# Kernel optimization log

Hardware: AMD Instinct MI355X
Metric: run time of the kernel (lower is better)

Reference implementation:

```python
import jax, jax.numpy as jnp
import numpy as np

DIST_THD = 2.0  # squared-distance threshold from my_chamfer_fn


def setup_inputs() -> dict:
    key = jax.random.key(0)
    k1, k2 = jax.random.split(key)
    pc1 = jax.random.normal(k1, (1, 16384, 3), dtype=jnp.float32)
    pc2 = jax.random.normal(k2, (1, 16384, 3), dtype=jnp.float32)
    return {"pc1": pc1, "pc2": pc2}


def _chamfer(x, y):
    # x: (N, P1, D), y: (N, P2, D). Squared pairwise distances (as pytorch3d knn_points).
    x2 = jnp.sum(x * x, axis=-1)                       # (N, P1)
    y2 = jnp.sum(y * y, axis=-1)                       # (N, P2)
    xy = jnp.einsum('npd,nqd->npq', x, y)              # (N, P1, P2)
    d2 = x2[:, :, None] + y2[:, None, :] - 2.0 * xy    # (N, P1, P2)
    cham_x = jnp.min(d2, axis=2)                       # (N, P1) NN dist x->y (K=1)
    cham_y = jnp.min(d2, axis=1)                       # (N, P2) NN dist y->x
    # threshold mask: distances >= 2 are zeroed
    cham_x = jnp.where(cham_x >= DIST_THD, 0.0, cham_x)
    cham_y = jnp.where(cham_y >= DIST_THD, 0.0, cham_y)
    N, P1, _ = x.shape
    P2 = y.shape[1]
    # point_reduction='mean' (lengths are full P), batch_reduction='mean'
    cx = jnp.sum(cham_x, axis=1) / P1
    cy = jnp.sum(cham_y, axis=1) / P2
    return jnp.sum(cx) / N + jnp.sum(cy) / N


def reference(pc1, pc2):
    # Chamfer loss between pc1 and pc2 (the kernel inside NSFP optimization);
    # normals are unused in this code path, so only the distance loss is returned.
    return _chamfer(pc1, pc2)
```

## Files before the change

### kernel.cpp

```cpp
#include <hip/hip_runtime.h>
#include <hip/hip_bf16.h>


constexpr int P      = 16384;
constexpr int BLK    = 256;
constexpr int NSEG   = 16;
constexpr int SEGPTS = P / NSEG;
constexpr int SEGT   = SEGPTS / 32;
constexpr int ROWSB  = 256;
constexpr int CLOUDB = P * 32;

typedef short s8v  __attribute__((ext_vector_type(8)));
typedef float f16v __attribute__((ext_vector_type(16)));

static __device__ inline unsigned short bf16r(float f) {
    unsigned u = __float_as_uint(f);
    u = (u + 0x7FFFu + ((u >> 16) & 1u)) >> 16;
    return (unsigned short)u;
}
static __device__ inline float bf2f(unsigned short h) {
    return __uint_as_float(((unsigned)h) << 16);
}

static __device__ inline void encA(float a, float b, float c, unsigned e[8]) {
    const unsigned ONE = 0x3F80u;
    const float s = fmaf(a, a, fmaf(b, b, c * c));
    const unsigned short ah = bf16r(a), bh = bf16r(b), ch = bf16r(c);
    const unsigned short al = bf16r(a - bf2f(ah));
    const unsigned short bl = bf16r(b - bf2f(bh));
    const unsigned short cl = bf16r(c - bf2f(ch));
    const unsigned short sh = bf16r(s), sl = bf16r(s - bf2f(sh));
    e[0] = ah | ((unsigned)al << 16);
    e[1] = bh | ((unsigned)bl << 16);
    e[2] = ch | ((unsigned)cl << 16);
    e[3] = ah | ((unsigned)bh << 16);
    e[4] = ch | ((unsigned)sh << 16);
    e[5] = sl | (ONE << 16);
    e[6] = ONE;
    e[7] = 0;
}

static __device__ inline void encB(float a, float b, float c, unsigned e[8]) {
    const unsigned ONE = 0x3F80u;
    const float s = fmaf(a, a, fmaf(b, b, c * c));
    const unsigned short ah = bf16r(a), bh = bf16r(b), ch = bf16r(c);
    const unsigned short al = bf16r(a - bf2f(ah));
    const unsigned short bl = bf16r(b - bf2f(bh));
    const unsigned short cl = bf16r(c - bf2f(ch));
    const unsigned short sh = bf16r(s), sl = bf16r(s - bf2f(sh));
    const unsigned short Ah = bf16r(-2.f * bf2f(ah)), Bh = bf16r(-2.f * bf2f(bh));
    const unsigned short Ch = bf16r(-2.f * bf2f(ch));
    const unsigned short Al = bf16r(-2.f * bf2f(al)), Bl = bf16r(-2.f * bf2f(bl));
    const unsigned short Cl = bf16r(-2.f * bf2f(cl));
    e[0] = Ah | ((unsigned)Ah << 16);
    e[1] = Bh | ((unsigned)Bh << 16);
    e[2] = Ch | ((unsigned)Ch << 16);
    e[3] = Al | ((unsigned)Bl << 16);
    e[4] = Cl | (ONE << 16);
    e[5] = ONE | ((unsigned)sh << 16);
    e[6] = sl;
    e[7] = 0;
}

__global__ __launch_bounds__(BLK) void encode_pts(
    const float* __restrict__ pc1, const float* __restrict__ pc2,
    unsigned char* __restrict__ encAbuf, unsigned char* __restrict__ encBbuf,
    float* __restrict__ out)
{
    const int gid = blockIdx.x * BLK + threadIdx.x;
    if (gid == 0) out[0] = 0.0f;
    const int c = gid >> 14;
    const int p = gid & (P - 1);
    const float* src = c ? pc2 : pc1;
    const float x = src[3 * p], y = src[3 * p + 1], z = src[3 * p + 2];

    unsigned ea[8], eb[8];
    encA(x, y, z, ea);
    encB(x, y, z, eb);

    unsigned char* ap = encAbuf + (size_t)c * CLOUDB + (size_t)p * 32;
    *(uint4*)(ap)      = make_uint4(ea[0], ea[1], ea[2], ea[3]);
    *(uint4*)(ap + 16) = make_uint4(ea[4], ea[5], ea[6], ea[7]);

    unsigned char* bp = encBbuf + (size_t)c * CLOUDB + (size_t)(p >> 5) * 1024
                        + (size_t)(p & 31) * 16;
    *(uint4*)(bp)       = make_uint4(eb[0], eb[1], eb[2], eb[3]);
    *(uint4*)(bp + 512) = make_uint4(eb[4], eb[5], eb[6], eb[7]);
}

__global__ __launch_bounds__(BLK, 4) void chamfer_mfma(
    const unsigned char* __restrict__ encAbuf,
    const unsigned char* __restrict__ encBbuf,
    float* __restrict__ part)
{
    const int dir = blockIdx.z;
    const int acloud = dir;
    const int bcloud = dir ^ 1;

    const int tid  = threadIdx.x;
    const int lane = tid & 63;
    const int wv   = tid >> 6;
    const int l31  = lane & 31;
    const int half = lane >> 5;

    const int rowbase = blockIdx.x * ROWSB + wv * 64;
    const unsigned char* abase = encAbuf + (size_t)acloud * CLOUDB + (size_t)half * 16;
    const s8v afrag0 = *(const s8v*)(abase + (size_t)(rowbase + l31) * 32);
    const s8v afrag1 = *(const s8v*)(abase + (size_t)(rowbase + 32 + l31) * 32);

    f16v acc0, acc1, Z;
    #pragma unroll
    for (int i = 0; i < 16; ++i) { acc0[i] = 3.0e38f; acc1[i] = 3.0e38f; Z[i] = 0.0f; }

    const unsigned char* bp = encBbuf + (size_t)bcloud * CLOUDB
                              + (size_t)(blockIdx.y * SEGPTS) * 32
                              + (size_t)lane * 16;
    #pragma unroll 4
    for (int t = 0; t < SEGT; t += 2, bp += 2048) {
        const s8v b0 = *(const s8v*)(bp);
        const s8v b1 = *(const s8v*)(bp + 1024);
        {
            const f16v da = __builtin_amdgcn_mfma_f32_32x32x16_bf16(afrag0, b0, Z, 0, 0, 0);
            const f16v db = __builtin_amdgcn_mfma_f32_32x32x16_bf16(afrag0, b1, Z, 0, 0, 0);
            #pragma unroll
            for (int i = 0; i < 16; ++i)
                acc0[i] = fminf(acc0[i], fminf(da[i], db[i]));
        }
        {
            const f16v da = __builtin_amdgcn_mfma_f32_32x32x16_bf16(afrag1, b0, Z, 0, 0, 0);
            const f16v db = __builtin_amdgcn_mfma_f32_32x32x16_bf16(afrag1, b1, Z, 0, 0, 0);
            #pragma unroll
            for (int i = 0; i < 16; ++i)
                acc1[i] = fminf(acc1[i], fminf(da[i], db[i]));
        }
    }

    float* pbase = part + ((size_t)(dir * NSEG + blockIdx.y)) * P;
    #pragma unroll
    for (int s = 0; s < 2; ++s) {
        #pragma unroll
        for (int rg = 0; rg < 16; ++rg) {
            float v = s ? acc1[rg] : acc0[rg];
            v = fminf(v, __shfl_xor(v, 1, 64));
            v = fminf(v, __shfl_xor(v, 2, 64));
            v = fminf(v, __shfl_xor(v, 4, 64));
            v = fminf(v, __shfl_xor(v, 8, 64));
            v = fminf(v, __shfl_xor(v, 16, 64));
            if (l31 == 0) {
                const int row = rowbase + s * 32 + (rg & 3) + 8 * (rg >> 2) + 4 * half;
                pbase[row] = v;
            }
        }
    }
}

__global__ __launch_bounds__(BLK) void chamfer_reduce(
    const float* __restrict__ part, float* __restrict__ out)
{
    const int gid = blockIdx.x * BLK + threadIdx.x;
    const int dirbase = (gid >= P) ? NSEG * P : 0;
    const int row = gid & (P - 1);

    float m = part[dirbase + row];
    #pragma unroll
    for (int s = 1; s < NSEG; ++s) m = fminf(m, part[dirbase + s * P + row]);

    if (m >= 2.0f) m = 0.0f;
    float v = m * (1.0f / (float)P);

    #pragma unroll
    for (int off = 32; off > 0; off >>= 1) v += __shfl_down(v, off, 64);

    __shared__ float wsum[BLK / 64];
    const int lane = threadIdx.x & 63;
    const int wvi = threadIdx.x >> 6;
    if (lane == 0) wsum[wvi] = v;
    __syncthreads();
    if (threadIdx.x == 0) {
        float ssum = wsum[0];
        #pragma unroll
        for (int w = 1; w < BLK / 64; ++w) ssum += wsum[w];
        atomicAdd(out, ssum);
    }
}

extern "C" void kernel_launch(void* const* d_in, const int* in_sizes, int n_in,
                              void* d_out, int out_size, void* d_ws, size_t ws_size,
                              hipStream_t stream) {
    const float* pc1 = (const float*)d_in[0];
    const float* pc2 = (const float*)d_in[1];
    float* out = (float*)d_out;
    unsigned char* ws = (unsigned char*)d_ws;
    float* part = (float*)ws;
    unsigned char* encBbuf = ws + (2u << 20);
    unsigned char* encAbuf = ws + (3u << 20);

    encode_pts<<<(2 * P) / BLK, BLK, 0, stream>>>(pc1, pc2, encAbuf, encBbuf, out);

    dim3 grid(P / ROWSB, NSEG, 2);
    chamfer_mfma<<<grid, BLK, 0, stream>>>(encAbuf, encBbuf, part);
    chamfer_reduce<<<(2 * P) / BLK, BLK, 0, stream>>>(part, out);
}
```

Before: 104.2 us.

## Switch chamfer distance MFMA from 32x32x16 to 16x16x32 tiles with padded encodings

Replaces the 32x32x16 bf16 MFMA with the 16x16x32 variant. Point encodings are zero-padded to 64 bytes so the K dimension fits, and the B buffer becomes a plain row layout. Rows per block, the number of segments and the occupancy hint are retuned to match, and the workspace offsets shift. This aims for smaller accumulators and higher occupancy, but each useful distance now costs more MFMA work because half of K is zero padding.

Measured after the change: 123.4 us. 1.18x slower.

```diff
diff --git a/kernel.cpp b/kernel.cpp
--- a/kernel.cpp
+++ b/kernel.cpp
@@ -2,16 +2,15 @@
 #include <hip/hip_bf16.h>
 
 
-constexpr int P      = 16384;
-constexpr int BLK    = 256;
-constexpr int NSEG   = 16;
-constexpr int SEGPTS = P / NSEG;
-constexpr int SEGT   = SEGPTS / 32;
-constexpr int ROWSB  = 256;
-constexpr int CLOUDB = P * 32;
-
-typedef short s8v  __attribute__((ext_vector_type(8)));
-typedef float f16v __attribute__((ext_vector_type(16)));
+constexpr int P       = 16384;
+constexpr int BLK     = 256;
+constexpr int NSEG    = 8;
+constexpr int SEGPTS  = P / NSEG;
+constexpr int ROWSB   = 128;
+constexpr int CLOUDB  = P * 64;
+
+typedef short s8v __attribute__((ext_vector_type(8)));
+typedef float f4v __attribute__((ext_vector_type(4)));
 
 static __device__ inline unsigned short bf16r(float f) {
     unsigned u = __float_as_uint(f);
@@ -77,18 +76,22 @@
     unsigned ea[8], eb[8];
     encA(x, y, z, ea);
     encB(x, y, z, eb);
-
-    unsigned char* ap = encAbuf + (size_t)c * CLOUDB + (size_t)p * 32;
+    const uint4 zero = make_uint4(0, 0, 0, 0);
+
+    unsigned char* ap = encAbuf + (size_t)c * CLOUDB + (size_t)p * 64;
     *(uint4*)(ap)      = make_uint4(ea[0], ea[1], ea[2], ea[3]);
     *(uint4*)(ap + 16) = make_uint4(ea[4], ea[5], ea[6], ea[7]);
-
-    unsigned char* bp = encBbuf + (size_t)c * CLOUDB + (size_t)(p >> 5) * 1024
-                        + (size_t)(p & 31) * 16;
-    *(uint4*)(bp)       = make_uint4(eb[0], eb[1], eb[2], eb[3]);
-    *(uint4*)(bp + 512) = make_uint4(eb[4], eb[5], eb[6], eb[7]);
-}
-
-__global__ __launch_bounds__(BLK, 4) void chamfer_mfma(
+    *(uint4*)(ap + 32) = zero;
+    *(uint4*)(ap + 48) = zero;
+
+    unsigned char* bp = encBbuf + (size_t)c * CLOUDB + (size_t)p * 64;
+    *(uint4*)(bp)      = make_uint4(eb[0], eb[1], eb[2], eb[3]);
+    *(uint4*)(bp + 16) = make_uint4(eb[4], eb[5], eb[6], eb[7]);
+    *(uint4*)(bp + 32) = zero;
+    *(uint4*)(bp + 48) = zero;
+}
+
+__global__ __launch_bounds__(BLK, 6) void chamfer_mfma(
     const unsigned char* __restrict__ encAbuf,
     const unsigned char* __restrict__ encBbuf,
     float* __restrict__ part)
@@ -100,54 +103,50 @@
     const int tid  = threadIdx.x;
     const int lane = tid & 63;
     const int wv   = tid >> 6;
-    const int l31  = lane & 31;
-    const int half = lane >> 5;
-
-    const int rowbase = blockIdx.x * ROWSB + wv * 64;
-    const unsigned char* abase = encAbuf + (size_t)acloud * CLOUDB + (size_t)half * 16;
-    const s8v afrag0 = *(const s8v*)(abase + (size_t)(rowbase + l31) * 32);
-    const s8v afrag1 = *(const s8v*)(abase + (size_t)(rowbase + 32 + l31) * 32);
-
-    f16v acc0, acc1, Z;
-    #pragma unroll
-    for (int i = 0; i < 16; ++i) { acc0[i] = 3.0e38f; acc1[i] = 3.0e38f; Z[i] = 0.0f; }
+    const int l15  = lane & 15;
+    const int kg   = lane >> 4;
+
+    const int rowbase = blockIdx.x * ROWSB + wv * 32;
+    const unsigned char* abase = encAbuf + (size_t)acloud * CLOUDB
+                                 + (size_t)kg * 16;
+    const s8v a0 = *(const s8v*)(abase + (size_t)(rowbase + l15) * 64);
+    const s8v a1 = *(const s8v*)(abase + (size_t)(rowbase + 16 + l15) * 64);
+
+    f4v acc0, acc1, Z;
+    #pragma unroll
+    for (int i = 0; i < 4; ++i) { acc0[i] = 3.0e38f; acc1[i] = 3.0e38f; Z[i] = 0.0f; }
 
     const unsigned char* bp = encBbuf + (size_t)bcloud * CLOUDB
-                              + (size_t)(blockIdx.y * SEGPTS) * 32
-                              + (size_t)lane * 16;
+                              + (size_t)(blockIdx.y * SEGPTS) * 64
+                              + (size_t)l15 * 64 + (size_t)kg * 16;
     #pragma unroll 4
-    for (int t = 0; t < SEGT; t += 2, bp += 2048) {
+    for (int t = 0; t < SEGPTS / 16; t += 2, bp += 2048) {
         const s8v b0 = *(const s8v*)(bp);
         const s8v b1 = *(const s8v*)(bp + 1024);
-        {
-            const f16v da = __builtin_amdgcn_mfma_f32_32x32x16_bf16(afrag0, b0, Z, 0, 0, 0);
-            const f16v db = __builtin_amdgcn_mfma_f32_32x32x16_bf16(afrag0, b1, Z, 0, 0, 0);
-            #pragma unroll
-            for (int i = 0; i < 16; ++i)
-                acc0[i] = fminf(acc0[i], fminf(da[i], db[i]));
-        }
-        {
-            const f16v da = __builtin_amdgcn_mfma_f32_32x32x16_bf16(afrag1, b0, Z, 0, 0, 0);
-            const f16v db = __builtin_amdgcn_mfma_f32_32x32x16_bf16(afrag1, b1, Z, 0, 0, 0);
-            #pragma unroll
-            for (int i = 0; i < 16; ++i)
-                acc1[i] = fminf(acc1[i], fminf(da[i], db[i]));
-        }
+        const f4v d0a = __builtin_amdgcn_mfma_f32_16x16x32_bf16(a0, b0, Z, 0, 0, 0);
+        const f4v d0b = __builtin_amdgcn_mfma_f32_16x16x32_bf16(a0, b1, Z, 0, 0, 0);
+        #pragma unroll
+        for (int i = 0; i < 4; ++i)
+            acc0[i] = fminf(acc0[i], fminf(d0a[i], d0b[i]));
+        const f4v d1a = __builtin_amdgcn_mfma_f32_16x16x32_bf16(a1, b0, Z, 0, 0, 0);
+        const f4v d1b = __builtin_amdgcn_mfma_f32_16x16x32_bf16(a1, b1, Z, 0, 0, 0);
+        #pragma unroll
+        for (int i = 0; i < 4; ++i)
+            acc1[i] = fminf(acc1[i], fminf(d1a[i], d1b[i]));
     }
 
     float* pbase = part + ((size_t)(dir * NSEG + blockIdx.y)) * P;
     #pragma unroll
     for (int s = 0; s < 2; ++s) {
         #pragma unroll
-        for (int rg = 0; rg < 16; ++rg) {
-            float v = s ? acc1[rg] : acc0[rg];
+        for (int i = 0; i < 4; ++i) {
+            float v = s ? acc1[i] : acc0[i];
             v = fminf(v, __shfl_xor(v, 1, 64));
             v = fminf(v, __shfl_xor(v, 2, 64));
             v = fminf(v, __shfl_xor(v, 4, 64));
             v = fminf(v, __shfl_xor(v, 8, 64));
-            v = fminf(v, __shfl_xor(v, 16, 64));
-            if (l31 == 0) {
-                const int row = rowbase + s * 32 + (rg & 3) + 8 * (rg >> 2) + 4 * half;
+            if (l15 == 0) {
+                const int row = rowbase + s * 16 + kg * 4 + i;
                 pbase[row] = v;
             }
         }
@@ -192,7 +191,7 @@
     float* out = (float*)d_out;
     unsigned char* ws = (unsigned char*)d_ws;
     float* part = (float*)ws;
-    unsigned char* encBbuf = ws + (2u << 20);
+    unsigned char* encBbuf = ws + (1u << 20);
     unsigned char* encAbuf = ws + (3u << 20);
 
     encode_pts<<<(2 * P) / BLK, BLK, 0, stream>>>(pc1, pc2, encAbuf, encBbuf, out);
```

## Double-buffer B fragments in registers, halve segments, XCD-aware block mapping

Applied to the files above, without the earlier changes.

The chamfer MFMA kernel now loads B fragments into two register buffers of eight fragments each and alternates between them, so global loads for the next group are issued while MFMAs run on the current group. The number of B segments drops from 16 to 8, which doubles the work per block and halves the partial-min buffer. The grid is flattened to 1024 blocks with an explicit mapping that places each (direction, segment) combination on a particular XCD so that its B segment stays in one L2. The occupancy hint in launch bounds is removed, which raises register pressure and may lower occupancy.

New measurement: 136.3 us. +30.8%, slower.

```diff
diff --git a/kernel.cpp b/kernel.cpp
--- a/kernel.cpp
+++ b/kernel.cpp
@@ -4,9 +4,8 @@
 
 constexpr int P      = 16384;
 constexpr int BLK    = 256;
-constexpr int NSEG   = 16;
+constexpr int NSEG   = 8;
 constexpr int SEGPTS = P / NSEG;
-constexpr int SEGT   = SEGPTS / 32;
 constexpr int ROWSB  = 256;
 constexpr int CLOUDB = P * 32;
 
@@ -88,12 +87,19 @@
     *(uint4*)(bp + 512) = make_uint4(eb[4], eb[5], eb[6], eb[7]);
 }
 
-__global__ __launch_bounds__(BLK, 4) void chamfer_mfma(
+__global__ __launch_bounds__(BLK) void chamfer_mfma(
     const unsigned char* __restrict__ encAbuf,
     const unsigned char* __restrict__ encBbuf,
     float* __restrict__ part)
 {
-    const int dir = blockIdx.z;
+    const int wgid  = blockIdx.x;
+    const int xcd   = wgid & 7;
+    const int slot  = wgid >> 3;
+    const int combo = xcd * 2 + (slot >> 6);
+    const int bx    = slot & 63;
+    const int seg   = combo & 7;
+    const int dir   = combo >> 3;
+
     const int acloud = dir;
     const int bcloud = dir ^ 1;
 
@@ -103,7 +109,7 @@
     const int l31  = lane & 31;
     const int half = lane >> 5;
 
-    const int rowbase = blockIdx.x * ROWSB + wv * 64;
+    const int rowbase = bx * ROWSB + wv * 64;
     const unsigned char* abase = encAbuf + (size_t)acloud * CLOUDB + (size_t)half * 16;
     const s8v afrag0 = *(const s8v*)(abase + (size_t)(rowbase + l31) * 32);
     const s8v afrag1 = *(const s8v*)(abase + (size_t)(rowbase + 32 + l31) * 32);
@@ -113,29 +119,45 @@
     for (int i = 0; i < 16; ++i) { acc0[i] = 3.0e38f; acc1[i] = 3.0e38f; Z[i] = 0.0f; }
 
     const unsigned char* bp = encBbuf + (size_t)bcloud * CLOUDB
-                              + (size_t)(blockIdx.y * SEGPTS) * 32
+                              + (size_t)(seg * SEGPTS) * 32
                               + (size_t)lane * 16;
-    #pragma unroll 4
-    for (int t = 0; t < SEGT; t += 2, bp += 2048) {
-        const s8v b0 = *(const s8v*)(bp);
-        const s8v b1 = *(const s8v*)(bp + 1024);
-        {
-            const f16v da = __builtin_amdgcn_mfma_f32_32x32x16_bf16(afrag0, b0, Z, 0, 0, 0);
-            const f16v db = __builtin_amdgcn_mfma_f32_32x32x16_bf16(afrag0, b1, Z, 0, 0, 0);
+
+    auto compute = [&](const s8v* X) {
+        #pragma unroll
+        for (int k = 0; k < 8; k += 2) {
+            const f16v d0a = __builtin_amdgcn_mfma_f32_32x32x16_bf16(afrag0, X[k],     Z, 0, 0, 0);
+            const f16v d0b = __builtin_amdgcn_mfma_f32_32x32x16_bf16(afrag0, X[k + 1], Z, 0, 0, 0);
             #pragma unroll
             for (int i = 0; i < 16; ++i)
-                acc0[i] = fminf(acc0[i], fminf(da[i], db[i]));
-        }
-        {
-            const f16v da = __builtin_amdgcn_mfma_f32_32x32x16_bf16(afrag1, b0, Z, 0, 0, 0);
-            const f16v db = __builtin_amdgcn_mfma_f32_32x32x16_bf16(afrag1, b1, Z, 0, 0, 0);
+                acc0[i] = fminf(acc0[i], fminf(d0a[i], d0b[i]));
+            const f16v d1a = __builtin_amdgcn_mfma_f32_32x32x16_bf16(afrag1, X[k],     Z, 0, 0, 0);
+            const f16v d1b = __builtin_amdgcn_mfma_f32_32x32x16_bf16(afrag1, X[k + 1], Z, 0, 0, 0);
             #pragma unroll
             for (int i = 0; i < 16; ++i)
-                acc1[i] = fminf(acc1[i], fminf(da[i], db[i]));
+                acc1[i] = fminf(acc1[i], fminf(d1a[i], d1b[i]));
         }
+    };
+
+    s8v Abuf[8], Bbuf[8];
+    #pragma unroll
+    for (int k = 0; k < 8; ++k)
+        Abuf[k] = *(const s8v*)(bp + k * 1024);
+
+    #pragma unroll 1
+    for (int g = 0; g < 8; g += 2) {
+        #pragma unroll
+        for (int k = 0; k < 8; ++k)
+            Bbuf[k] = *(const s8v*)(bp + ((g + 1) * 8 + k) * 1024);
+        compute(Abuf);
+        if (g + 2 < 8) {
+            #pragma unroll
+            for (int k = 0; k < 8; ++k)
+                Abuf[k] = *(const s8v*)(bp + ((g + 2) * 8 + k) * 1024);
+        }
+        compute(Bbuf);
     }
 
-    float* pbase = part + ((size_t)(dir * NSEG + blockIdx.y)) * P;
+    float* pbase = part + ((size_t)(dir * NSEG + seg)) * P;
     #pragma unroll
     for (int s = 0; s < 2; ++s) {
         #pragma unroll
@@ -192,12 +214,11 @@
     float* out = (float*)d_out;
     unsigned char* ws = (unsigned char*)d_ws;
     float* part = (float*)ws;
-    unsigned char* encBbuf = ws + (2u << 20);
-    unsigned char* encAbuf = ws + (3u << 20);
+    unsigned char* encBbuf = ws + (1u << 20);
+    unsigned char* encAbuf = ws + (2u << 20);
 
     encode_pts<<<(2 * P) / BLK, BLK, 0, stream>>>(pc1, pc2, encAbuf, encBbuf, out);
 
-    dim3 grid(P / ROWSB, NSEG, 2);
-    chamfer_mfma<<<grid, BLK, 0, stream>>>(encAbuf, encBbuf, part);
+    chamfer_mfma<<<dim3(1024), BLK, 0, stream>>>(encAbuf, encBbuf, part);
     chamfer_reduce<<<(2 * P) / BLK, BLK, 0, stream>>>(part, out);
 }
```
